# Performance work log

Hardware: AMD Instinct MI355X
Metric: run time of the kernel (lower is better)

The kernel has to match this reference:

```python
import jax, jax.numpy as jnp
import numpy as np

DIM = 512
HEADS = 8
HEAD_DIM = DIM // HEADS
K = 16
SCALE = HEAD_DIM ** -0.5
EPS = 1e-5


def _layer_norm(x, g, b):
    mu = jnp.mean(x, axis=-1, keepdims=True)
    var = jnp.mean(jnp.square(x - mu), axis=-1, keepdims=True)
    return (x - mu) * jax.lax.rsqrt(var + EPS) * g + b


def setup_inputs() -> dict:
    key = jax.random.key(0)
    ks = jax.random.split(key, 16)
    D = DIM
    s = D ** -0.5
    x = jax.random.normal(ks[0], (2, 4096, D), dtype=jnp.float32)
    p = {
        'x': x,
        'q_w': jax.random.normal(ks[1], (D, D), jnp.float32) * s,
        'q_b': jnp.zeros((D,), jnp.float32),
        'k_w': jax.random.normal(ks[2], (D, D), jnp.float32) * s,
        'k_b': jnp.zeros((D,), jnp.float32),
        'v_w': jax.random.normal(ks[3], (D, D), jnp.float32) * s,
        'v_b': jnp.zeros((D,), jnp.float32),
        'o_w': jax.random.normal(ks[4], (D, D), jnp.float32) * s,
        'o_b': jnp.zeros((D,), jnp.float32),
        'ln1_g': jnp.ones((D,), jnp.float32),
        'ln1_b': jnp.zeros((D,), jnp.float32),
        'ln2_g': jnp.ones((D,), jnp.float32),
        'ln2_b': jnp.zeros((D,), jnp.float32),
        'ff1_w': jax.random.normal(ks[5], (D, 4 * D), jnp.float32) * s,
        'ff1_b': jnp.zeros((4 * D,), jnp.float32),
        'ff2_w': jax.random.normal(ks[6], (4 * D, D), jnp.float32) * (4 * D) ** -0.5,
        'ff2_b': jnp.zeros((D,), jnp.float32),
    }
    return p


def reference(x, q_w, q_b, k_w, k_b, v_w, v_b, o_w, o_b,
              ln1_g, ln1_b, ln2_g, ln2_b, ff1_w, ff1_b, ff2_w, ff2_b):
    B, N, D = x.shape
    residual = x
    xn = _layer_norm(x, ln1_g, ln1_b)
    Q = (xn @ q_w + q_b).reshape(B, N, HEADS, HEAD_DIM)
    Kt = (xn @ k_w + k_b).reshape(B, N, HEADS, HEAD_DIM)
    V = (xn @ v_w + v_b).reshape(B, N, HEADS, HEAD_DIM)
    # dense scores [B,H,N,N]
    logits = jnp.einsum('bnhd,bmhd->bhnm', Q, Kt) * SCALE
    topk_vals, topk_idx = jax.lax.top_k(logits, K)  # [B,H,N,K]
    # softmax over only the top-k entries == scatter(-inf) + dense softmax
    attn = jax.nn.softmax(topk_vals, axis=-1)
    Vh = V.transpose(0, 2, 1, 3)  # [B,H,M,hd]
    # gather V rows at top-k indices -> [B,H,N,K,hd]
    Vg = jnp.take_along_axis(Vh[:, :, None, :, :], topk_idx[..., None], axis=3)
    out = jnp.einsum('bhnk,bhnkd->bnhd', attn, Vg).reshape(B, N, D)
    out = out @ o_w + o_b
    x2 = residual + out
    h = _layer_norm(x2, ln2_g, ln2_b)
    ff = jax.nn.gelu(h @ ff1_w + ff1_b, approximate=False) @ ff2_w + ff2_b
    return x2 + ff
```

## Files before the change

### kernel.cpp

```cpp
#include <hip/hip_runtime.h>
#include <math.h>

#define DIMD 512
#define NSEQ 4096
#define NHEAD 8
#define HD 64
#define TOPK 16

__global__ __launch_bounds__(256) void ln_stats_kernel(
    const float* __restrict__ X, float2* __restrict__ S)
{
    int r = blockIdx.x;
    int t = threadIdx.x;
    const float* xr = X + (size_t)r * DIMD;
    float a = xr[t], b = xr[t + 256];
    float s = a + b;
    float sq = a * a + b * b;
    #pragma unroll
    for (int off = 32; off > 0; off >>= 1) {
        s  += __shfl_down(s, off, 64);
        sq += __shfl_down(sq, off, 64);
    }
    __shared__ float red[8];
    int wv = t >> 6, ln = t & 63;
    if (ln == 0) { red[wv] = s; red[wv + 4] = sq; }
    __syncthreads();
    if (t == 0) {
        float st  = red[0] + red[1] + red[2] + red[3];
        float sqt = red[4] + red[5] + red[6] + red[7];
        float mean = st * (1.0f / DIMD);
        float var  = sqt * (1.0f / DIMD) - mean * mean;
        float inv  = 1.0f / sqrtf(var + 1e-5f);
        S[r] = make_float2(mean, inv);
    }
}

__global__ __launch_bounds__(256) void gemm_f32(
    const float* __restrict__ A, const float* __restrict__ W,
    const float* __restrict__ bias, const float* __restrict__ R,
    float* __restrict__ C, int Kd, int Nn, int gelu,
    const float2* __restrict__ lnstats,
    const float* __restrict__ lng, const float* __restrict__ lnb)
{
    __shared__ float As[32][64];
    __shared__ float Ws[32][64];
    int n0 = blockIdx.x * 64;
    int m0 = blockIdx.y * 64;
    int t  = threadIdx.x;
    int tr = t >> 4, tc = t & 15;
    float acc[4][4] = {};

    for (int k0 = 0; k0 < Kd; k0 += 32) {
        #pragma unroll
        for (int qq = 0; qq < 2; ++qq) {
            int idx = t * 2 + qq;
            int r   = idx >> 3;
            int c4  = idx & 7;
            float4 av = *(const float4*)&A[(size_t)(m0 + r) * Kd + k0 + c4 * 4];
            if (lnstats) {
                float2 st = lnstats[m0 + r];
                float4 gv = *(const float4*)&lng[k0 + c4 * 4];
                float4 bv = *(const float4*)&lnb[k0 + c4 * 4];
                av.x = (av.x - st.x) * st.y * gv.x + bv.x;
                av.y = (av.y - st.x) * st.y * gv.y + bv.y;
                av.z = (av.z - st.x) * st.y * gv.z + bv.z;
                av.w = (av.w - st.x) * st.y * gv.w + bv.w;
            }
            As[c4 * 4 + 0][r] = av.x;
            As[c4 * 4 + 1][r] = av.y;
            As[c4 * 4 + 2][r] = av.z;
            As[c4 * 4 + 3][r] = av.w;
            int kr  = idx >> 4;
            int nc4 = idx & 15;
            *(float4*)&Ws[kr][nc4 * 4] =
                *(const float4*)&W[(size_t)(k0 + kr) * Nn + n0 + nc4 * 4];
        }
        __syncthreads();
        #pragma unroll
        for (int kk = 0; kk < 32; ++kk) {
            float4 a = *(const float4*)&As[kk][tr * 4];
            float4 b = *(const float4*)&Ws[kk][tc * 4];
            acc[0][0] += a.x * b.x; acc[0][1] += a.x * b.y;
            acc[0][2] += a.x * b.z; acc[0][3] += a.x * b.w;
            acc[1][0] += a.y * b.x; acc[1][1] += a.y * b.y;
            acc[1][2] += a.y * b.z; acc[1][3] += a.y * b.w;
            acc[2][0] += a.z * b.x; acc[2][1] += a.z * b.y;
            acc[2][2] += a.z * b.z; acc[2][3] += a.z * b.w;
            acc[3][0] += a.w * b.x; acc[3][1] += a.w * b.y;
            acc[3][2] += a.w * b.z; acc[3][3] += a.w * b.w;
        }
        __syncthreads();
    }

    float4 bb = *(const float4*)&bias[n0 + tc * 4];
    #pragma unroll
    for (int i = 0; i < 4; ++i) {
        int row = m0 + tr * 4 + i;
        float4 o;
        o.x = acc[i][0] + bb.x;
        o.y = acc[i][1] + bb.y;
        o.z = acc[i][2] + bb.z;
        o.w = acc[i][3] + bb.w;
        if (gelu) {
            o.x = 0.5f * o.x * (1.0f + erff(o.x * 0.70710678118654752f));
            o.y = 0.5f * o.y * (1.0f + erff(o.y * 0.70710678118654752f));
            o.z = 0.5f * o.z * (1.0f + erff(o.z * 0.70710678118654752f));
            o.w = 0.5f * o.w * (1.0f + erff(o.w * 0.70710678118654752f));
        }
        if (R) {
            float4 rv = *(const float4*)&R[(size_t)row * Nn + n0 + tc * 4];
            o.x += rv.x; o.y += rv.y; o.z += rv.z; o.w += rv.w;
        }
        *(float4*)&C[(size_t)row * Nn + n0 + tc * 4] = o;
    }
}

#define INSERT_SLOT(SLOTV, SLOTI)                                        \
    {                                                                    \
        unsigned long long lt = __ballot(SLOTV < scb);                   \
        int cnt = __popcll((lt >> (gg * 16)) & 0xFFFFull);               \
        if (cnt) {                                                       \
            float shv = __shfl(SLOTV, (lane + 1) & 63);                  \
            int   shi = __shfl(SLOTI, (lane + 1) & 63);                  \
            bool put = ing && (s == cnt - 1);                            \
            bool shf = ing && (s < cnt - 1);                             \
            SLOTV = put ? scb : (shf ? shv : SLOTV);                     \
            SLOTI = put ? idxb : (shf ? shi : SLOTI);                    \
        }                                                                \
    }

__global__ __launch_bounds__(512, 4) void topk_attn_fused(
    const float* __restrict__ Qm, const float* __restrict__ Km,
    const float* __restrict__ Vm, float* __restrict__ Om)
{
    __shared__ float4 Ks4[64 * 16];
    __shared__ float4 Qs4[64 * 16];

    int bid = blockIdx.x;
    int bh  = bid >> 6;
    int qt  = bid & 63;
    int b   = bh >> 3, h = bh & 7;
    int qbase = qt * 64;
    int tid  = threadIdx.x;
    int wid  = __builtin_amdgcn_readfirstlane(tid >> 6);
    int lane = tid & 63;
    int grp  = lane >> 4;
    int s    = lane & 15;

    size_t kbase = ((size_t)b * NSEQ) * DIMD + h * HD;

    #pragma unroll
    for (int qq = 0; qq < 2; ++qq) {
        int idx = tid * 2 + qq;
        int r   = idx >> 4;
        int c4  = idx & 15;
        Qs4[r * 16 + c4] = *(const float4*)
            &Qm[((size_t)(b * NSEQ + qbase + r)) * DIMD + h * HD + c4 * 4];
    }

    float slotvA = -INFINITY, slotvB = -INFINITY;
    int   slotiA = 0,         slotiB = 0;

    for (int t0 = 0; t0 < NSEQ; t0 += 64) {
        __syncthreads();
        #pragma unroll
        for (int qq = 0; qq < 2; ++qq) {
            int idx = tid * 2 + qq;
            int r   = idx >> 4;
            int c4  = idx & 15;
            Ks4[r * 16 + (c4 ^ (r & 15))] =
                *(const float4*)&Km[kbase + (size_t)(t0 + r) * DIMD + c4 * 4];
        }
        __syncthreads();

        float a0[8], a1[8], a2[8], a3[8];
        #pragma unroll
        for (int g = 0; g < 8; ++g) { a0[g] = a1[g] = a2[g] = a3[g] = 0.f; }
        #pragma unroll 4
        for (int d4 = 0; d4 < 16; ++d4) {
            float4 kv = Ks4[lane * 16 + (d4 ^ (lane & 15))];
            #pragma unroll
            for (int g = 0; g < 8; ++g) {
                float4 qv = Qs4[(wid * 8 + g) * 16 + d4];
                a0[g] = fmaf(qv.x, kv.x, a0[g]);
                a1[g] = fmaf(qv.y, kv.y, a1[g]);
                a2[g] = fmaf(qv.z, kv.z, a2[g]);
                a3[g] = fmaf(qv.w, kv.w, a3[g]);
            }
        }

        #pragma unroll
        for (int g = 0; g < 8; ++g) {
            float sc = ((a0[g] + a1[g]) + (a2[g] + a3[g])) * 0.125f;
            int gg = g & 3;
            bool ing = (grp == gg);
            float theta = __shfl((g < 4) ? slotvA : slotvB, gg * 16);
            unsigned long long cand = __ballot(sc > theta);
            while (cand) {
                int src = __ffsll(cand) - 1;
                cand &= cand - 1;
                float scb  = __shfl(sc, src);
                int   idxb = t0 + src;
                if (g < 4) INSERT_SLOT(slotvA, slotiA)
                else       INSERT_SLOT(slotvB, slotiB)
            }
        }
    }

    #pragma unroll
    for (int set = 0; set < 2; ++set) {
        float slotv = set ? slotvB : slotvA;
        int   sloti = set ? slotiB : slotiA;
        float mx = __shfl(slotv, (lane & 48) + 15);
        float w  = expf(slotv - mx);
        float ssum = w;
        #pragma unroll
        for (int off = 1; off < 16; off <<= 1) ssum += __shfl_xor(ssum, off);
        float wn = w * (1.0f / ssum);

        #pragma unroll
        for (int gg2 = 0; gg2 < 4; ++gg2) {
            float acc = 0.f;
            #pragma unroll
            for (int i = 15; i >= 0; --i) {
                float wi = __shfl(wn, gg2 * 16 + i);
                int   ki = __shfl(sloti, gg2 * 16 + i);
                acc = fmaf(wi, Vm[((size_t)(b * NSEQ + ki)) * DIMD + h * HD + lane], acc);
            }
            int qn = qbase + wid * 8 + set * 4 + gg2;
            Om[((size_t)(b * NSEQ + qn)) * DIMD + h * HD + lane] = acc;
        }
    }
}

extern "C" void kernel_launch(void* const* d_in, const int* in_sizes, int n_in,
                              void* d_out, int out_size, void* d_ws, size_t ws_size,
                              hipStream_t stream)
{
    (void)in_sizes; (void)n_in; (void)out_size; (void)ws_size;
    const float* x    = (const float*)d_in[0];
    const float* q_w  = (const float*)d_in[1];
    const float* q_b  = (const float*)d_in[2];
    const float* k_w  = (const float*)d_in[3];
    const float* k_b  = (const float*)d_in[4];
    const float* v_w  = (const float*)d_in[5];
    const float* v_b  = (const float*)d_in[6];
    const float* o_w  = (const float*)d_in[7];
    const float* o_b  = (const float*)d_in[8];
    const float* ln1g = (const float*)d_in[9];
    const float* ln1b = (const float*)d_in[10];
    const float* ln2g = (const float*)d_in[11];
    const float* ln2b = (const float*)d_in[12];
    const float* ff1w = (const float*)d_in[13];
    const float* ff1b = (const float*)d_in[14];
    const float* ff2w = (const float*)d_in[15];
    const float* ff2b = (const float*)d_in[16];
    float* out = (float*)d_out;
    float* ws  = (float*)d_ws;

    const size_t SZ = (size_t)8192 * DIMD;
    float*  Qb      = ws;
    float*  Kb      = ws + SZ;
    float*  Vb      = ws + 2 * SZ;
    float*  attnOut = ws + 3 * SZ;
    float2* stats   = (float2*)(ws + 4 * SZ);
    float*  ffb     = ws;

    dim3 g512(8, 128);

    ln_stats_kernel<<<8192, 256, 0, stream>>>(x, stats);
    gemm_f32<<<g512, 256, 0, stream>>>(x, q_w, q_b, nullptr, Qb,
                                       512, 512, 0, stats, ln1g, ln1b);
    gemm_f32<<<g512, 256, 0, stream>>>(x, k_w, k_b, nullptr, Kb,
                                       512, 512, 0, stats, ln1g, ln1b);
    gemm_f32<<<g512, 256, 0, stream>>>(x, v_w, v_b, nullptr, Vb,
                                       512, 512, 0, stats, ln1g, ln1b);

    topk_attn_fused<<<1024, 512, 0, stream>>>(Qb, Kb, Vb, attnOut);

    gemm_f32<<<g512, 256, 0, stream>>>(attnOut, o_w, o_b, x, out,
                                       512, 512, 0, nullptr, nullptr, nullptr);

    ln_stats_kernel<<<8192, 256, 0, stream>>>(out, stats);
    gemm_f32<<<dim3(32, 128), 256, 0, stream>>>(out, ff1w, ff1b, nullptr, ffb,
                                                512, 2048, 1, stats, ln2g, ln2b);
    gemm_f32<<<g512, 256, 0, stream>>>(ffb, ff2w, ff2b, out, out,
                                       2048, 512, 0, nullptr, nullptr, nullptr);
}
```

Baseline: 1.967 ms.

## Transpose K to head-major layout and drop LDS staging in top-k attention

Adds a transpose kernel that writes K as [b,h,d,n] into the output buffer used as scratch. The attention kernel then reads K directly from global memory with coalesced per-lane loads and reads Q via wave-uniform scalar addresses, removing the shared-memory tiles and the two barriers per key tile. Launch bounds occupancy hint drops from 4 to 2. This trades LDS traffic and synchronisation for more global/L2 loads and an extra kernel pass, and may raise register pressure.

```diff
diff --git a/kernel.cpp b/kernel.cpp
--- a/kernel.cpp
+++ b/kernel.cpp
@@ -115,6 +115,39 @@
     }
 }
 
+__global__ __launch_bounds__(256) void transpose_k(
+    const float* __restrict__ Kb, float* __restrict__ Kt)
+{
+    __shared__ float tile[64][65];
+    int bid = blockIdx.x;
+    int nt = bid & 63;
+    int h  = (bid >> 6) & 7;
+    int b  = bid >> 9;
+    int n0 = nt * 64;
+    int t  = threadIdx.x;
+    int r  = t >> 2;
+    int cg = t & 3;
+
+    #pragma unroll
+    for (int j = 0; j < 4; ++j) {
+        int c = (cg + 4 * j) * 4;
+        float4 v = *(const float4*)
+            &Kb[(size_t)(b * 4096 + n0 + r) * DIMD + h * HD + c];
+        tile[r][c + 0] = v.x; tile[r][c + 1] = v.y;
+        tile[r][c + 2] = v.z; tile[r][c + 3] = v.w;
+    }
+    __syncthreads();
+    int d = t >> 2;
+    #pragma unroll
+    for (int j = 0; j < 4; ++j) {
+        int nc = (cg + 4 * j) * 4;
+        float4 o;
+        o.x = tile[nc + 0][d]; o.y = tile[nc + 1][d];
+        o.z = tile[nc + 2][d]; o.w = tile[nc + 3][d];
+        *(float4*)&Kt[((size_t)((b * 8 + h) * HD + d)) * NSEQ + n0 + nc] = o;
+    }
+}
+
 #define INSERT_SLOT(SLOTV, SLOTI)                                        \
     {                                                                    \
         unsigned long long lt = __ballot(SLOTV < scb);                   \
@@ -129,13 +162,10 @@
         }                                                                \
     }
 
-__global__ __launch_bounds__(512, 4) void topk_attn_fused(
-    const float* __restrict__ Qm, const float* __restrict__ Km,
+__global__ __launch_bounds__(512, 2) void topk_attn_fused(
+    const float* __restrict__ Qm, const float* __restrict__ Kt,
     const float* __restrict__ Vm, float* __restrict__ Om)
 {
-    __shared__ float4 Ks4[64 * 16];
-    __shared__ float4 Qs4[64 * 16];
-
     int bid = blockIdx.x;
     int bh  = bid >> 6;
     int qt  = bid & 63;
@@ -147,45 +177,39 @@
     int grp  = lane >> 4;
     int s    = lane & 15;
 
-    size_t kbase = ((size_t)b * NSEQ) * DIMD + h * HD;
-
-    #pragma unroll
-    for (int qq = 0; qq < 2; ++qq) {
-        int idx = tid * 2 + qq;
-        int r   = idx >> 4;
-        int c4  = idx & 15;
-        Qs4[r * 16 + c4] = *(const float4*)
-            &Qm[((size_t)(b * NSEQ + qbase + r)) * DIMD + h * HD + c4 * 4];
-    }
+    const float* qrow0 = Qm + ((size_t)(b * NSEQ + qbase + wid * 8)) * DIMD + h * HD;
+    const float* ktb   = Kt + ((size_t)bh * HD) * NSEQ;
 
     float slotvA = -INFINITY, slotvB = -INFINITY;
     int   slotiA = 0,         slotiB = 0;
 
     for (int t0 = 0; t0 < NSEQ; t0 += 64) {
-        __syncthreads();
-        #pragma unroll
-        for (int qq = 0; qq < 2; ++qq) {
-            int idx = tid * 2 + qq;
-            int r   = idx >> 4;
-            int c4  = idx & 15;
-            Ks4[r * 16 + (c4 ^ (r & 15))] =
-                *(const float4*)&Km[kbase + (size_t)(t0 + r) * DIMD + c4 * 4];
-        }
-        __syncthreads();
-
+        const float* kp = ktb + t0 + lane;
         float a0[8], a1[8], a2[8], a3[8];
         #pragma unroll
         for (int g = 0; g < 8; ++g) { a0[g] = a1[g] = a2[g] = a3[g] = 0.f; }
-        #pragma unroll 4
-        for (int d4 = 0; d4 < 16; ++d4) {
-            float4 kv = Ks4[lane * 16 + (d4 ^ (lane & 15))];
+
+        #pragma unroll
+        for (int c = 0; c < 8; ++c) {
+            float k0 = kp[(size_t)(8 * c + 0) * NSEQ];
+            float k1 = kp[(size_t)(8 * c + 1) * NSEQ];
+            float k2 = kp[(size_t)(8 * c + 2) * NSEQ];
+            float k3 = kp[(size_t)(8 * c + 3) * NSEQ];
+            float k4 = kp[(size_t)(8 * c + 4) * NSEQ];
+            float k5 = kp[(size_t)(8 * c + 5) * NSEQ];
+            float k6 = kp[(size_t)(8 * c + 6) * NSEQ];
+            float k7 = kp[(size_t)(8 * c + 7) * NSEQ];
             #pragma unroll
             for (int g = 0; g < 8; ++g) {
-                float4 qv = Qs4[(wid * 8 + g) * 16 + d4];
-                a0[g] = fmaf(qv.x, kv.x, a0[g]);
-                a1[g] = fmaf(qv.y, kv.y, a1[g]);
-                a2[g] = fmaf(qv.z, kv.z, a2[g]);
-                a3[g] = fmaf(qv.w, kv.w, a3[g]);
+                const float* qp = qrow0 + (size_t)g * DIMD + 8 * c;
+                a0[g] = fmaf(qp[0], k0, a0[g]);
+                a1[g] = fmaf(qp[1], k1, a1[g]);
+                a2[g] = fmaf(qp[2], k2, a2[g]);
+                a3[g] = fmaf(qp[3], k3, a3[g]);
+                a0[g] = fmaf(qp[4], k4, a0[g]);
+                a1[g] = fmaf(qp[5], k5, a1[g]);
+                a2[g] = fmaf(qp[6], k6, a2[g]);
+                a3[g] = fmaf(qp[7], k7, a3[g]);
             }
         }
 
@@ -265,6 +289,7 @@
     float*  attnOut = ws + 3 * SZ;
     float2* stats   = (float2*)(ws + 4 * SZ);
     float*  ffb     = ws;
+    float*  Kt      = out;
 
     dim3 g512(8, 128);
 
@@ -276,7 +301,8 @@
     gemm_f32<<<g512, 256, 0, stream>>>(x, v_w, v_b, nullptr, Vb,
                                        512, 512, 0, stats, ln1g, ln1b);
 
-    topk_attn_fused<<<1024, 512, 0, stream>>>(Qb, Kb, Vb, attnOut);
+    transpose_k<<<1024, 256, 0, stream>>>(Kb, Kt);
+    topk_attn_fused<<<1024, 512, 0, stream>>>(Qb, Kt, Vb, attnOut);
 
     gemm_f32<<<g512, 256, 0, stream>>>(attnOut, o_w, o_b, x, out,
                                        512, 512, 0, nullptr, nullptr, nullptr);
```

Measured after the change: 2.297 ms. 16.8% more time.

## Register-block two keys per lane and stream half the Q rows from global

Applied to the files above, without the earlier changes.

The key tile grows from 64 to 128 rows, so each lane computes scores for two keys at once and every Q value read is reused across both. Half of the Q rows per wave (g>=4) are now read straight from global memory at wave-uniform addresses instead of from LDS, which cuts LDS read traffic. Tile loads are also re-indexed for coalescing, and the occupancy hint in launch_bounds is dropped. In exchange, register pressure roughly doubles in the accumulators, which may lower occupancy, and the second candidate batch is filtered against a threshold read before the first batch is inserted.

```diff
diff --git a/kernel.cpp b/kernel.cpp
--- a/kernel.cpp
+++ b/kernel.cpp
@@ -122,18 +122,18 @@
         if (cnt) {                                                       \
             float shv = __shfl(SLOTV, (lane + 1) & 63);                  \
             int   shi = __shfl(SLOTI, (lane + 1) & 63);                  \
-            bool put = ing && (s == cnt - 1);                            \
-            bool shf = ing && (s < cnt - 1);                             \
+            bool put = ing && (sl == cnt - 1);                           \
+            bool shf = ing && (sl < cnt - 1);                            \
             SLOTV = put ? scb : (shf ? shv : SLOTV);                     \
             SLOTI = put ? idxb : (shf ? shi : SLOTI);                    \
         }                                                                \
     }
 
-__global__ __launch_bounds__(512, 4) void topk_attn_fused(
+__global__ __launch_bounds__(512) void topk_attn_fused(
     const float* __restrict__ Qm, const float* __restrict__ Km,
     const float* __restrict__ Vm, float* __restrict__ Om)
 {
-    __shared__ float4 Ks4[64 * 16];
+    __shared__ float4 Ks4[128 * 16];
     __shared__ float4 Qs4[64 * 16];
 
     int bid = blockIdx.x;
@@ -145,27 +145,33 @@
     int wid  = __builtin_amdgcn_readfirstlane(tid >> 6);
     int lane = tid & 63;
     int grp  = lane >> 4;
-    int s    = lane & 15;
+    int sl   = lane & 15;
 
     size_t kbase = ((size_t)b * NSEQ) * DIMD + h * HD;
 
     #pragma unroll
     for (int qq = 0; qq < 2; ++qq) {
-        int idx = tid * 2 + qq;
+        int idx = tid + 512 * qq;
         int r   = idx >> 4;
         int c4  = idx & 15;
         Qs4[r * 16 + c4] = *(const float4*)
             &Qm[((size_t)(b * NSEQ + qbase + r)) * DIMD + h * HD + c4 * 4];
     }
 
+    const float* qrow0 = Qm + ((size_t)(b * NSEQ + qbase + wid * 8)) * DIMD + h * HD;
+    const float* qb4 = qrow0 + 4 * DIMD;
+    const float* qb5 = qrow0 + 5 * DIMD;
+    const float* qb6 = qrow0 + 6 * DIMD;
+    const float* qb7 = qrow0 + 7 * DIMD;
+
     float slotvA = -INFINITY, slotvB = -INFINITY;
     int   slotiA = 0,         slotiB = 0;
 
-    for (int t0 = 0; t0 < NSEQ; t0 += 64) {
+    for (int t0 = 0; t0 < NSEQ; t0 += 128) {
         __syncthreads();
         #pragma unroll
-        for (int qq = 0; qq < 2; ++qq) {
-            int idx = tid * 2 + qq;
+        for (int qq = 0; qq < 4; ++qq) {
+            int idx = tid + 512 * qq;
             int r   = idx >> 4;
             int c4  = idx & 15;
             Ks4[r * 16 + (c4 ^ (r & 15))] =
@@ -173,34 +179,59 @@
         }
         __syncthreads();
 
-        float a0[8], a1[8], a2[8], a3[8];
-        #pragma unroll
-        for (int g = 0; g < 8; ++g) { a0[g] = a1[g] = a2[g] = a3[g] = 0.f; }
-        #pragma unroll 4
+        float a0A[8], a1A[8], a2A[8], a3A[8];
+        float a0B[8], a1B[8], a2B[8], a3B[8];
+        #pragma unroll
+        for (int g = 0; g < 8; ++g) {
+            a0A[g] = a1A[g] = a2A[g] = a3A[g] = 0.f;
+            a0B[g] = a1B[g] = a2B[g] = a3B[g] = 0.f;
+        }
+
+        #pragma unroll
         for (int d4 = 0; d4 < 16; ++d4) {
-            float4 kv = Ks4[lane * 16 + (d4 ^ (lane & 15))];
+            float4 kvA = Ks4[lane * 16 + (d4 ^ (lane & 15))];
+            float4 kvB = Ks4[(lane + 64) * 16 + (d4 ^ (lane & 15))];
             #pragma unroll
             for (int g = 0; g < 8; ++g) {
-                float4 qv = Qs4[(wid * 8 + g) * 16 + d4];
-                a0[g] = fmaf(qv.x, kv.x, a0[g]);
-                a1[g] = fmaf(qv.y, kv.y, a1[g]);
-                a2[g] = fmaf(qv.z, kv.z, a2[g]);
-                a3[g] = fmaf(qv.w, kv.w, a3[g]);
+                float4 qv;
+                if (g < 4)      qv = Qs4[(wid * 8 + g) * 16 + d4];
+                else if (g == 4) qv = *(const float4*)(qb4 + 4 * d4);
+                else if (g == 5) qv = *(const float4*)(qb5 + 4 * d4);
+                else if (g == 6) qv = *(const float4*)(qb6 + 4 * d4);
+                else             qv = *(const float4*)(qb7 + 4 * d4);
+                a0A[g] = fmaf(qv.x, kvA.x, a0A[g]);
+                a1A[g] = fmaf(qv.y, kvA.y, a1A[g]);
+                a2A[g] = fmaf(qv.z, kvA.z, a2A[g]);
+                a3A[g] = fmaf(qv.w, kvA.w, a3A[g]);
+                a0B[g] = fmaf(qv.x, kvB.x, a0B[g]);
+                a1B[g] = fmaf(qv.y, kvB.y, a1B[g]);
+                a2B[g] = fmaf(qv.z, kvB.z, a2B[g]);
+                a3B[g] = fmaf(qv.w, kvB.w, a3B[g]);
             }
         }
 
         #pragma unroll
         for (int g = 0; g < 8; ++g) {
-            float sc = ((a0[g] + a1[g]) + (a2[g] + a3[g])) * 0.125f;
+            float scA = ((a0A[g] + a1A[g]) + (a2A[g] + a3A[g])) * 0.125f;
+            float scB = ((a0B[g] + a1B[g]) + (a2B[g] + a3B[g])) * 0.125f;
             int gg = g & 3;
             bool ing = (grp == gg);
             float theta = __shfl((g < 4) ? slotvA : slotvB, gg * 16);
-            unsigned long long cand = __ballot(sc > theta);
-            while (cand) {
-                int src = __ffsll(cand) - 1;
-                cand &= cand - 1;
-                float scb  = __shfl(sc, src);
+            unsigned long long candA = __ballot(scA > theta);
+            unsigned long long candB = __ballot(scB > theta);
+            while (candA) {
+                int src = __ffsll(candA) - 1;
+                candA &= candA - 1;
+                float scb  = __shfl(scA, src);
                 int   idxb = t0 + src;
+                if (g < 4) INSERT_SLOT(slotvA, slotiA)
+                else       INSERT_SLOT(slotvB, slotiB)
+            }
+            while (candB) {
+                int src = __ffsll(candB) - 1;
+                candB &= candB - 1;
+                float scb  = __shfl(scB, src);
+                int   idxb = t0 + 64 + src;
                 if (g < 4) INSERT_SLOT(slotvA, slotiA)
                 else       INSERT_SLOT(slotvB, slotiB)
             }
```

New measurement: 7.857 ms. 3.99x slower.
